# Kernel tuning notes

Hardware: AMD Instinct MI355X
Metric: run time of the kernel (lower is better)

## Reference

```python
import math
import jax, jax.numpy as jnp
import numpy as np

B, N1, N2 = 4, 1024, 768
DIM, H, DK = 1536, 8, 64
DV = DIM // H          # 192
NRPF = DIM // H        # 192, divisible by 6
ESM_CELL = 1280 + 256  # 1536
LN_EPS = 1e-5


def layer_norm(t, g, b):
    mu = jnp.mean(t, axis=-1, keepdims=True)
    var = jnp.mean(jnp.square(t - mu), axis=-1, keepdims=True)
    return (t - mu) * jax.lax.rsqrt(var + LN_EPS) * g + b


def positional_embed(n, feature_size):
    # Enformer-style relative positional features for distances -n+1..n-1
    distances = jnp.arange(-n + 1, n, dtype=jnp.float32)  # [2n-1]
    absd = jnp.abs(distances)[:, None]
    nb = feature_size // 6  # 3 basis fns x 2 (sym + signed)
    seq_len = float(n)
    # exponential
    max_range = math.log(seq_len) / math.log(2.0)
    half_life = 2.0 ** jnp.linspace(3.0, max_range, nb)
    f_exp = jnp.exp(-math.log(2.0) / half_life * absd)
    # central mask
    widths = 2.0 ** jnp.arange(1, nb + 1, dtype=jnp.float32) - 1.0
    f_cm = (widths[None, :] > absd).astype(jnp.float32)
    # gamma pdf
    stddev = seq_len / (2.0 * nb)
    start_mean = seq_len / nb
    mean = jnp.linspace(start_mean, seq_len, nb)
    conc = (mean / stddev) ** 2
    rate = mean / stddev ** 2
    log_p = jax.scipy.special.xlogy(conc - 1.0, absd) - rate * absd
    log_norm = jax.scipy.special.gammaln(conc) - conc * jnp.log(rate)
    prob = jnp.exp(log_p - log_norm) + 1e-8
    f_gam = prob / jnp.max(prob, axis=-1, keepdims=True)
    emb = jnp.concatenate([f_exp, f_cm, f_gam], axis=-1)
    return jnp.concatenate([emb, jnp.sign(distances)[:, None] * emb], axis=-1)  # [2n-1, feature_size]


def relative_shift(x):
    # x: [b, h, t1, 2n-1] -> [b, h, t1, n]
    b, h, t1, _ = x.shape
    x = jnp.pad(x, ((0, 0), (0, 0), (0, 0), (1, 0)))
    t2 = x.shape[-1]  # 2n
    x = x.reshape(b, h, t2, t1)[:, :, 1:, :].reshape(b, h, t1, t2 - 1)
    return x[..., : (t2 + 1) // 2]


def ffn(t, g, b, w1, b1, w2, b2):
    h = layer_norm(t, g, b)
    h = jax.nn.relu(h @ w1 + b1)
    return h @ w2 + b2


def setup_inputs() -> dict:
    key = jax.random.key(0)
    ks = jax.random.split(key, 20)
    s = 0.02
    d = {
        'x': jax.random.normal(ks[0], (B, N1, DIM), jnp.float32),
        'y0': jax.random.normal(ks[1], (B, N2, ESM_CELL), jnp.float32),
        'res_w': jax.random.normal(ks[2], (ESM_CELL, DIM)) * s,
        'lnx_g': jnp.ones((DIM,)), 'lnx_b': jnp.zeros((DIM,)),
        'lny_g': jnp.ones((DIM,)), 'lny_b': jnp.zeros((DIM,)),
        'wq': jax.random.normal(ks[3], (DIM, H * DK)) * s,
        'wk': jax.random.normal(ks[4], (DIM, H * DK)) * s,
        'wv1': jax.random.normal(ks[5], (DIM, H * DV)) * s,
        'wv2': jax.random.normal(ks[6], (DIM, H * DV)) * s,
        'wrel': jax.random.normal(ks[7], (NRPF, H * DK)) * s,
        'rel_pos_bias': jax.random.normal(ks[8], (1, H, 1, DK)),
        'wo1': jax.random.normal(ks[9], (H * DV, DIM)) * s, 'bo1': jnp.zeros((DIM,)),
        'wo2': jax.random.normal(ks[10], (H * DV, DIM)) * s, 'bo2': jnp.zeros((DIM,)),
        'fx_ln_g': jnp.ones((DIM,)), 'fx_ln_b': jnp.zeros((DIM,)),
        'fx_w1': jax.random.normal(ks[11], (DIM, 2 * DIM)) * s, 'fx_b1': jnp.zeros((2 * DIM,)),
        'fx_w2': jax.random.normal(ks[12], (2 * DIM, DIM)) * s, 'fx_b2': jnp.zeros((DIM,)),
        'fy_ln_g': jnp.ones((DIM,)), 'fy_ln_b': jnp.zeros((DIM,)),
        'fy_w1': jax.random.normal(ks[13], (DIM, 2 * DIM)) * s, 'fy_b1': jnp.zeros((2 * DIM,)),
        'fy_w2': jax.random.normal(ks[14], (2 * DIM, DIM)) * s, 'fy_b2': jnp.zeros((DIM,)),
    }
    return d


def reference(x, y0, res_w, lnx_g, lnx_b, lny_g, lny_b, wq, wk, wv1, wv2,
              wrel, rel_pos_bias, wo1, bo1, wo2, bo2,
              fx_ln_g, fx_ln_b, fx_w1, fx_b1, fx_w2, fx_b2,
              fy_ln_g, fy_ln_b, fy_w1, fy_b1, fy_w2, fy_b2):
    scale = DK ** -0.5
    y = y0 @ res_w                                   # res_proj (first layer)
    x1 = layer_norm(x, lnx_g, lnx_b)
    y1 = layer_norm(y, lny_g, lny_b)

    def heads(t, dh):  # [b, n, h*dh] -> [b, h, n, dh]
        return t.reshape(t.shape[0], t.shape[1], H, dh).transpose(0, 2, 1, 3)

    q = heads(x1 @ wq, DK) * scale                   # [b,h,n1,dk]
    k = heads(y1 @ wk, DK)                           # [b,h,n2,dk]
    v2 = heads(y1 @ wv2, DV)                         # [b,h,n2,dv]

    content = jnp.einsum('bhid,bhjd->bhij', q, k)    # [b,h,n1,n2]

    pos = positional_embed(N1, NRPF)                 # [2n1-1, nrpf]
    rel_q = (pos @ wrel).reshape(2 * N1 - 1, H, DK).transpose(1, 0, 2)  # [h,2n1-1,dk]
    rel_logits = jnp.einsum('bhjd,hnd->bhjn', k * scale + rel_pos_bias, rel_q)  # [b,h,n2,2n1-1]
    rel_logits = relative_shift(rel_logits)          # [b,h,n2,n1]
    logits = content + rel_logits.transpose(0, 1, 3, 2)

    attn = jax.nn.softmax(logits, axis=-1)           # [b,h,n1,n2]

    out1 = jnp.einsum('bhij,bhjd->bhid', attn, v2)   # [b,h,n1,dv]
    out1 = out1.transpose(0, 2, 1, 3).reshape(B, N1, H * DV)
    x2 = out1 @ wo1 + bo1

    # exchange branch: reuse attn^T on v1 from stream x
    v1 = heads(x1 @ wv1, DV)                         # [b,h,n1,dv]
    out2 = jnp.einsum('bhij,bhid->bhjd', attn, v1)   # [b,h,n2,dv]
    out2 = out2.transpose(0, 2, 1, 3).reshape(B, N2, H * DV)
    y2 = out2 @ wo2 + bo2

    x4 = x + x2
    x5 = x4 + ffn(x4, fx_ln_g, fx_ln_b, fx_w1, fx_b1, fx_w2, fx_b2)
    y4 = y + y2
    y5 = y4 + ffn(y4, fy_ln_g, fy_ln_b, fy_w1, fy_b1, fy_w2, fy_b2)
    return x5, y5
```

## Files before the change

### kernel.cpp

```cpp
#include <hip/hip_runtime.h>
#include <stdint.h>
#include <math.h>

typedef __attribute__((ext_vector_type(8))) short s8v;
typedef __attribute__((ext_vector_type(4))) short s4v;
typedef __attribute__((ext_vector_type(4))) float f4v;

#define DEV static __device__ __forceinline__

DEV short f2bf(float f) {
  uint32_t u = __builtin_bit_cast(uint32_t, f);
  u += 0x7FFFu + ((u >> 16) & 1u);
  return (short)(u >> 16);
}
DEV float bf2f(short s) {
  uint32_t u = ((uint32_t)(uint16_t)s) << 16;
  return __builtin_bit_cast(float, u);
}

#define GLD16(g, l) __builtin_amdgcn_global_load_lds( \
    (const __attribute__((address_space(1))) void*)(g), \
    (__attribute__((address_space(3))) void*)(l), 16, 0, 0)

__global__ __launch_bounds__(256) void gemm_bt(
    const short* __restrict__ A, const short* __restrict__ B,
    float* Cf, short* Cb,
    const float* __restrict__ bias, const float* resid,
    int M, int N, int K, int lda, int ldb, int ldc,
    long long sAo, long long sAi, long long sBo, long long sBi,
    long long sCo, long long sCi, float alpha, int relu)
{
  __shared__ __align__(16) short lA[128*32];
  __shared__ __align__(16) short lB[128*32];
  const int z = blockIdx.z, zo = z >> 3, zi = z & 7;
  const short* Ab = A + zo*sAo + zi*sAi;
  const short* Bb = B + zo*sBo + zi*sBi;
  const long long cOff = zo*sCo + zi*sCi;

  const int m0 = blockIdx.y*128, n0 = blockIdx.x*128;
  const int tid = threadIdx.x, lane = tid & 63, wv = tid >> 6;
  const int wm = (wv >> 1)*64, wn = (wv & 1)*64;
  const int fr = lane & 15, fq = lane >> 4;

  f4v acc[4][4] = {};

  const int rA0 = min(m0 + (tid >> 2), M - 1);
  const int rA1 = min(m0 + 64 + (tid >> 2), M - 1);
  const int rB0 = min(n0 + (tid >> 2), N - 1);
  const int rB1 = min(n0 + 64 + (tid >> 2), N - 1);
  const int pc = (tid & 3) * 8;
  const short* gA0 = Ab + (size_t)rA0*lda + pc;
  const short* gA1 = Ab + (size_t)rA1*lda + pc;
  const short* gB0 = Bb + (size_t)rB0*ldb + pc;
  const short* gB1 = Bb + (size_t)rB1*ldb + pc;
  short* dA0 = lA + (wv*64)*8;
  short* dA1 = lA + (256 + wv*64)*8;
  short* dB0 = lB + (wv*64)*8;
  short* dB1 = lB + (256 + wv*64)*8;

  for (int k0 = 0; k0 < K; k0 += 32) {
    GLD16(gA0 + k0, dA0);
    GLD16(gA1 + k0, dA1);
    GLD16(gB0 + k0, dB0);
    GLD16(gB1 + k0, dB1);
    __syncthreads();
    s8v af[4], bg[4];
#pragma unroll
    for (int i = 0; i < 4; i++) {
      af[i] = *(const s8v*)&lA[(wm + i*16 + fr)*32 + fq*8];
      bg[i] = *(const s8v*)&lB[(wn + i*16 + fr)*32 + fq*8];
    }
#pragma unroll
    for (int mi = 0; mi < 4; mi++)
#pragma unroll
      for (int ni = 0; ni < 4; ni++)
        acc[mi][ni] = __builtin_amdgcn_mfma_f32_16x16x32_bf16(af[mi], bg[ni], acc[mi][ni], 0, 0, 0);
    __syncthreads();
  }

#pragma unroll
  for (int mi = 0; mi < 4; mi++) {
    const int row = m0 + wm + mi*16 + fq*4;
#pragma unroll
    for (int ni = 0; ni < 4; ni++) {
      const int col = n0 + wn + ni*16 + fr;
      if (col >= N) continue;
      const float bv = bias ? bias[col] : 0.f;
#pragma unroll
      for (int r = 0; r < 4; r++) {
        if (row + r >= M) continue;
        float v = acc[mi][ni][r] * alpha + bv;
        const long long idx = cOff + (long long)(row + r)*ldc + col;
        if (resid) v += resid[idx];
        if (relu) v = fmaxf(v, 0.f);
        if (Cf) Cf[idx] = v;
        if (Cb) Cb[idx] = f2bf(v);
      }
    }
  }
}

#define ST_A(buf, ks, tt) do { const int ko = ((tt)<<6) + ((ks)<<5); \
    GLD16(gA0 + ko, ldA + ((buf)*2+(ks))*8192); \
    GLD16(gA1 + ko, ldA + ((buf)*2+(ks))*8192 + 4096); } while(0)
#define ST_B(buf, ks, tt) do { const int ko = ((tt)<<6) + ((ks)<<5); \
    GLD16(gB0 + ko, ldB + ((buf)*2+(ks))*8192); \
    GLD16(gB1 + ko, ldB + ((buf)*2+(ks))*8192 + 4096); } while(0)

#define PH256(buf, ks, mig, READB, DOWAIT, ...) do { \
    s8v av[4]; \
    const int rb = ((buf)*2+(ks))*8192; \
    _Pragma("unroll") for (int q2 = 0; q2 < 4; q2++) av[q2] = *(const s8v*)&smem[rb + aoff[(mig)*4+q2]]; \
    if (READB) { _Pragma("unroll") for (int q2 = 0; q2 < 4; q2++) bv[q2] = *(const s8v*)&smem[32768 + rb + boff[q2]]; } \
    __VA_ARGS__; \
    if (DOWAIT == 1) asm volatile("s_waitcnt vmcnt(6)" ::: "memory"); \
    if (DOWAIT == 2) asm volatile("s_waitcnt vmcnt(0)" ::: "memory"); \
    __builtin_amdgcn_s_barrier(); \
    asm volatile("s_waitcnt lgkmcnt(0)" ::: "memory"); \
    __builtin_amdgcn_s_setprio(1); \
    _Pragma("unroll") for (int q2 = 0; q2 < 4; q2++) \
      _Pragma("unroll") for (int u2 = 0; u2 < 4; u2++) \
        acc[(mig)*4+q2][u2] = __builtin_amdgcn_mfma_f32_16x16x32_bf16(av[q2], bv[u2], acc[(mig)*4+q2][u2], 0, 0, 0); \
    __builtin_amdgcn_s_setprio(0); \
  } while(0)

__global__ __launch_bounds__(512, 2) void gemm256(
    const short* __restrict__ A0p, const short* __restrict__ B0p,
    float* C0f, short* C0b, const float* __restrict__ bias0, const float* res0,
    int nb0, int nbm0, int N0, float al0,
    const short* __restrict__ A1p, const short* __restrict__ B1p,
    float* C1f, short* C1b, const float* __restrict__ bias1, const float* res1,
    int nbm1, int N1, float al1,
    int K, int relu)
{
  __shared__ __align__(16) short smem[65536];
  const int total = gridDim.x;
  int bid = blockIdx.x;
  if ((total & 7) == 0) bid = (bid & 7)*(total >> 3) + (bid >> 3);
  const short* A; const short* B; float* Cf; short* Cb; const float* bias; const float* resid;
  int tile, nbm, N; float alpha;
  if (bid < nb0) { A = A0p; B = B0p; Cf = C0f; Cb = C0b; bias = bias0; resid = res0;
                   tile = bid; nbm = nbm0; N = N0; alpha = al0; }
  else           { A = A1p; B = B1p; Cf = C1f; Cb = C1b; bias = bias1; resid = res1;
                   tile = bid - nb0; nbm = nbm1; N = N1; alpha = al1; }
  const int bm = tile % nbm, bn = tile / nbm;
  const int m0 = bm << 8, n0 = bn << 8;
  const int t = threadIdx.x, lane = t & 63, w = t >> 6;
  const int wm = w >> 2, wn = w & 3;
  const int fr = lane & 15, fq = lane >> 4;
  const int ntk = K >> 6;

  const int r0 = t >> 2, r1 = 128 + (t >> 2), gsw = t & 3;
  const int cs0 = (gsw ^ ((r0 >> 1) & 3)) << 3;
  const int cs1 = (gsw ^ ((r1 >> 1) & 3)) << 3;
  const short* gA0 = A + (size_t)(m0 + r0)*K + cs0;
  const short* gA1 = A + (size_t)(m0 + r1)*K + cs1;
  const short* gB0 = B + (size_t)(n0 + r0)*K + cs0;
  const short* gB1 = B + (size_t)(n0 + r1)*K + cs1;
  short* const ldA = smem + w*512;
  short* const ldB = smem + 32768 + w*512;

  int aoff[8], boff[4];
#pragma unroll
  for (int mi = 0; mi < 8; mi++) { const int r = wm*128 + mi*16 + fr; aoff[mi] = r*32 + ((fq ^ ((r >> 1) & 3)) << 3); }
#pragma unroll
  for (int ni = 0; ni < 4; ni++) { const int r = wn*64 + ni*16 + fr; boff[ni] = r*32 + ((fq ^ ((r >> 1) & 3)) << 3); }

  f4v acc[8][4] = {};
  s8v bv[4];

  ST_A(0,0,0); ST_B(0,0,0); ST_A(0,1,0); ST_B(0,1,0);
  ST_B(1,0,1); ST_A(1,0,1); ST_B(1,1,1);
  asm volatile("s_waitcnt vmcnt(6)" ::: "memory");
  __builtin_amdgcn_s_barrier();
  asm volatile("" ::: "memory");

  for (int it = 0, nit = (ntk >> 1) - 1; it < nit; ++it) {
    const int t1 = 2*it + 1, t2 = 2*it + 2, t3 = 2*it + 3;
    PH256(0,0,0, 1,0, ST_A(1,1,t1));
    PH256(0,0,1, 0,0, ST_B(0,0,t2));
    PH256(0,1,0, 1,0, ST_A(0,0,t2));
    PH256(0,1,1, 0,1, ST_B(0,1,t2));
    PH256(1,0,0, 1,0, ST_A(0,1,t2));
    PH256(1,0,1, 0,0, ST_B(1,0,t3));
    PH256(1,1,0, 1,0, ST_A(1,0,t3));
    PH256(1,1,1, 0,1, ST_B(1,1,t3));
  }
  PH256(0,0,0, 1,0, ST_A(1,1,ntk-1));
  PH256(0,0,1, 0,0, );
  PH256(0,1,0, 1,0, );
  PH256(0,1,1, 0,2, );
  PH256(1,0,0, 1,0, );
  PH256(1,0,1, 0,0, );
  PH256(1,1,0, 1,0, );
  PH256(1,1,1, 0,0, );

#pragma unroll
  for (int mi = 0; mi < 8; mi++) {
    const int row = m0 + wm*128 + mi*16 + fq*4;
#pragma unroll
    for (int ni = 0; ni < 4; ni++) {
      const int col = n0 + wn*64 + ni*16 + fr;
      const float bvv = bias ? bias[col] : 0.f;
#pragma unroll
      for (int r = 0; r < 4; r++) {
        float v = acc[mi][ni][r]*alpha + bvv;
        const size_t idx = (size_t)(row + r)*N + col;
        if (resid) v += resid[idx];
        if (relu) v = fmaxf(v, 0.f);
        if (Cf) Cf[idx] = v;
        else Cb[idx] = f2bf(v);
      }
    }
  }
}

__global__ __launch_bounds__(256) void wtrans(const float* __restrict__ src,
                                              short* __restrict__ dst, int R, int C)
{
  __shared__ float t[32][33];
  const int c0 = blockIdx.x*32, r0 = blockIdx.y*32;
  const int tx = threadIdx.x, ty = threadIdx.y;
#pragma unroll
  for (int k = 0; k < 4; k++)
    t[ty + k*8][tx] = src[(size_t)(r0 + ty + k*8)*C + c0 + tx];
  __syncthreads();
#pragma unroll
  for (int k = 0; k < 4; k++)
    dst[(size_t)(c0 + ty + k*8)*R + r0 + tx] = f2bf(t[tx][ty + k*8]);
}

__global__ __launch_bounds__(256) void btrans(const short* __restrict__ src, short* __restrict__ dst,
    int ls, int ld_, long long sSo, long long sSi, long long sDo, long long sDi)
{
  __shared__ short t[32][33];
  const int z = blockIdx.z;
  const short* S = src + (z>>3)*sSo + (z&7)*sSi;
  short* D = dst + (z>>3)*sDo + (z&7)*sDi;
  const int c0 = blockIdx.x*32, r0 = blockIdx.y*32;
  const int tx = threadIdx.x, ty = threadIdx.y;
#pragma unroll
  for (int k = 0; k < 4; k++)
    t[ty + k*8][tx] = S[(size_t)(r0 + ty + k*8)*ls + c0 + tx];
  __syncthreads();
#pragma unroll
  for (int k = 0; k < 4; k++)
    D[(size_t)(c0 + ty + k*8)*ld_ + r0 + tx] = t[tx][ty + k*8];
}

__global__ __launch_bounds__(256) void conv_bf(const float* __restrict__ src,
                                               short* __restrict__ dst, long long n)
{
  const long long i = ((long long)blockIdx.x*256 + threadIdx.x)*4;
  if (i >= n) return;
  const float4 v = *(const float4*)(src + i);
  s4v o = { f2bf(v.x), f2bf(v.y), f2bf(v.z), f2bf(v.w) };
  *(s4v*)(dst + i) = o;
}

__global__ __launch_bounds__(256) void ln_k(const float* __restrict__ in,
    const float* __restrict__ gam, const float* __restrict__ bet, short* __restrict__ out)
{
  const long long row = blockIdx.x;
  const float* r = in + row*1536;
  const int tid = threadIdx.x;
  float v[6], s = 0.f, s2 = 0.f;
#pragma unroll
  for (int i = 0; i < 6; i++) { v[i] = r[tid + i*256]; s += v[i]; s2 += v[i]*v[i]; }
  for (int m = 1; m < 64; m <<= 1) { s += __shfl_xor(s, m); s2 += __shfl_xor(s2, m); }
  __shared__ float rs[4], rs2[4];
  if ((tid & 63) == 0) { rs[tid>>6] = s; rs2[tid>>6] = s2; }
  __syncthreads();
  s = rs[0]+rs[1]+rs[2]+rs[3]; s2 = rs2[0]+rs2[1]+rs2[2]+rs2[3];
  const float mu  = s * (1.f/1536.f);
  const float var = s2 * (1.f/1536.f) - mu*mu;
  const float inv = rsqrtf(var + 1e-5f);
  short* o = out + row*1536;
#pragma unroll
  for (int i = 0; i < 6; i++) { int c = tid + i*256; o[c] = f2bf((v[i]-mu)*inv*gam[c] + bet[c]); }
}

__global__ __launch_bounds__(64) void posemb(short* __restrict__ out)
{
  const int i = blockIdx.x;
  const int j = threadIdx.x;
  const float dist = (float)(i - 1023);
  const float absd = fabsf(dist);
  float fe = 0.f, fc = 0.f, prob = 0.f;
  if (j < 32) {
    const float hl = exp2f(3.f + 7.f*(float)j/31.f);
    fe = expf(-0.6931471805599453f/hl * absd);
    const float width = exp2f((float)(j+1)) - 1.f;
    fc = (width > absd) ? 1.f : 0.f;
    const float m = 32.f*(float)(j+1);
    const float conc = (m/16.f)*(m/16.f);
    const float rate = m/256.f;
    const float logp = (absd > 0.f ? (conc-1.f)*logf(absd) : -INFINITY) - rate*absd;
    const float logn = lgammaf(conc) - conc*logf(rate);
    prob = expf(logp - logn) + 1e-8f;
  }
  float mx = prob;
  for (int m = 1; m < 32; m <<= 1) mx = fmaxf(mx, __shfl_xor(mx, m));
  if (j < 32) {
    const float fg = prob / mx;
    const float sg = dist > 0.f ? 1.f : (dist < 0.f ? -1.f : 0.f);
    const size_t base = (size_t)i*192;
    out[base + j]       = f2bf(fe);
    out[base + 32 + j]  = f2bf(fc);
    out[base + 64 + j]  = f2bf(fg);
    out[base + 96 + j]  = f2bf(sg*fe);
    out[base + 128 + j] = f2bf(sg*fc);
    out[base + 160 + j] = f2bf(sg*fg);
  }
}

__global__ __launch_bounds__(256) void relbias_k(const float* __restrict__ rpb,
    const short* __restrict__ relq, float* __restrict__ T)
{
  const int n = blockIdx.x;
  const int tid = threadIdx.x;
  const int h = tid >> 5, l = tid & 31;
  const int d = l*2;
  float s = rpb[h*64+d]   * bf2f(relq[(size_t)n*512 + h*64 + d])
          + rpb[h*64+d+1] * bf2f(relq[(size_t)n*512 + h*64 + d+1]);
  for (int m = 1; m < 32; m <<= 1) s += __shfl_xor(s, m);
  if (l == 0) T[h*2047 + n] = s;
}

__global__ __launch_bounds__(256) void scores_k(
    const short* __restrict__ qb, const short* __restrict__ kb,
    const short* __restrict__ relq, const float* __restrict__ T,
    float* __restrict__ L)
{
  __shared__ __align__(16) short smem[21504];
  short* kt  = smem;
  short* qt  = smem + 4608;
  short* rqt = smem + 4608;
  float* P   = (float*)(smem + 4608);

  const int z = blockIdx.z, b = z >> 3, h = z & 7;
  const int j0 = blockIdx.x*64, i0 = blockIdx.y*64;
  const int tid = threadIdx.x, lane = tid & 63, wv = tid >> 6;
  const int fr = lane & 15, fq = lane >> 4;

  {
    const short* kg = kb + (size_t)(b*768  + j0)*512 + h*64;
    const short* qg = qb + (size_t)(b*1024 + i0)*512 + h*64;
    for (int c = tid; c < 512; c += 256) {
      const int r = c >> 3, ch = (c & 7)*8;
      *(s8v*)&kt[r*72 + ch] = *(const s8v*)&kg[(size_t)r*512 + ch];
      *(s8v*)&qt[r*72 + ch] = *(const s8v*)&qg[(size_t)r*512 + ch];
    }
  }
  __syncthreads();

  const int wi = (wv & 1)*32, wj = (wv >> 1)*32;
  f4v c2[2][2] = {};
#pragma unroll
  for (int ks = 0; ks < 2; ks++) {
    s8v aq[2], bk[2];
#pragma unroll
    for (int mi = 0; mi < 2; mi++) aq[mi] = *(const s8v*)&qt[(wi + mi*16 + fr)*72 + ks*32 + fq*8];
#pragma unroll
    for (int ni = 0; ni < 2; ni++) bk[ni] = *(const s8v*)&kt[(wj + ni*16 + fr)*72 + ks*32 + fq*8];
#pragma unroll
    for (int mi = 0; mi < 2; mi++)
#pragma unroll
      for (int ni = 0; ni < 2; ni++)
        c2[mi][ni] = __builtin_amdgcn_mfma_f32_16x16x32_bf16(aq[mi], bk[ni], c2[mi][ni], 0, 0, 0);
  }
  __syncthreads();

  const int nbase = 704 + i0 - j0;
  {
    const short* rg = relq + (size_t)nbase*512 + h*64;
    for (int c = tid; c < 1024; c += 256) {
      const int r = c >> 3, ch = (c & 7)*8;
      *(s8v*)&rqt[r*72 + ch] = *(const s8v*)&rg[(size_t)r*512 + ch];
    }
  }
  __syncthreads();

  const int wj2 = (wv & 1)*32, wn2 = (wv >> 1)*64;
  f4v pr[2][4] = {};
#pragma unroll
  for (int ks = 0; ks < 2; ks++) {
    s8v a2[2], b2[4];
#pragma unroll
    for (int mi = 0; mi < 2; mi++) a2[mi] = *(const s8v*)&kt[(wj2 + mi*16 + fr)*72 + ks*32 + fq*8];
#pragma unroll
    for (int ni = 0; ni < 4; ni++) b2[ni] = *(const s8v*)&rqt[(wn2 + ni*16 + fr)*72 + ks*32 + fq*8];
#pragma unroll
    for (int mi = 0; mi < 2; mi++)
#pragma unroll
      for (int ni = 0; ni < 4; ni++)
        pr[mi][ni] = __builtin_amdgcn_mfma_f32_16x16x32_bf16(a2[mi], b2[ni], pr[mi][ni], 0, 0, 0);
  }
  __syncthreads();

#pragma unroll
  for (int mi = 0; mi < 2; mi++)
#pragma unroll
    for (int ni = 0; ni < 4; ni++)
#pragma unroll
      for (int r = 0; r < 4; r++)
        P[(wj2 + mi*16 + fq*4 + r)*132 + wn2 + ni*16 + fr] = pr[mi][ni][r];
  __syncthreads();

  const float* Tt = T + h*2047 + nbase;
  float* Lb = L + ((size_t)z*1024 + i0)*768 + j0;
#pragma unroll
  for (int mi = 0; mi < 2; mi++)
#pragma unroll
    for (int ni = 0; ni < 2; ni++)
#pragma unroll
      for (int r = 0; r < 4; r++) {
        const int il = wi + mi*16 + fq*4 + r;
        const int jl = wj + ni*16 + fr;
        const int nl = 63 + il - jl;
        Lb[(size_t)il*768 + jl] = c2[mi][ni][r] + 0.125f*P[jl*132 + nl] + Tt[nl];
      }
}

__global__ __launch_bounds__(256) void softmax_k(const float* __restrict__ L, short* __restrict__ P)
{
  const long long row = blockIdx.x;
  const float* r = L + row*768;
  const int tid = threadIdx.x;
  float v0 = r[tid], v1 = r[tid+256], v2 = r[tid+512];
  float mx = fmaxf(v0, fmaxf(v1, v2));
  for (int m = 1; m < 64; m <<= 1) mx = fmaxf(mx, __shfl_xor(mx, m));
  __shared__ float redm[4], reds[4];
  if ((tid & 63) == 0) redm[tid>>6] = mx;
  __syncthreads();
  mx = fmaxf(fmaxf(redm[0], redm[1]), fmaxf(redm[2], redm[3]));
  v0 = __expf(v0 - mx); v1 = __expf(v1 - mx); v2 = __expf(v2 - mx);
  float s = v0 + v1 + v2;
  for (int m = 1; m < 64; m <<= 1) s += __shfl_xor(s, m);
  if ((tid & 63) == 0) reds[tid>>6] = s;
  __syncthreads();
  s = reds[0] + reds[1] + reds[2] + reds[3];
  const float inv = 1.f / s;
  short* o = P + row*768;
  o[tid] = f2bf(v0*inv); o[tid+256] = f2bf(v1*inv); o[tid+512] = f2bf(v2*inv);
}

static void gemm(hipStream_t st, const short* A, const short* B, float* Cf, short* Cb,
                 const float* bias, const float* resid,
                 int M, int N, int K, int lda, int ldb, int ldc,
                 int batches = 1,
                 long long sAo = 0, long long sAi = 0, long long sBo = 0, long long sBi = 0,
                 long long sCo = 0, long long sCi = 0, float alpha = 1.f, int relu = 0)
{
  dim3 g((N + 127)/128, (M + 127)/128, batches);
  gemm_bt<<<g, dim3(256), 0, st>>>(A, B, Cf, Cb, bias, resid, M, N, K, lda, ldb, ldc,
                                   sAo, sAi, sBo, sBi, sCo, sCi, alpha, relu);
}

static void g256(hipStream_t st,
    const short* A0, const short* B0, float* C0f, short* C0b, const float* bias0, const float* res0,
    int M0, int N0, float al0,
    const short* A1, const short* B1, float* C1f, short* C1b, const float* bias1, const float* res1,
    int M1, int N1, float al1,
    int K, int relu)
{
  const int nbm0 = M0 >> 8, nbn0 = N0 >> 8, nb0 = nbm0*nbn0;
  const int nbm1 = M1 >> 8, nbn1 = N1 >> 8, nb1 = nbm1*nbn1;
  gemm256<<<dim3(nb0 + nb1), dim3(512), 0, st>>>(
      A0, B0, C0f, C0b, bias0, res0, nb0, nbm0, N0, al0,
      A1, B1, C1f, C1b, bias1, res1, nbm1, N1, al1, K, relu);
}

extern "C" void kernel_launch(void* const* d_in, const int* in_sizes, int n_in,
                              void* d_out, int out_size, void* d_ws, size_t ws_size,
                              hipStream_t stream)
{
  (void)in_sizes; (void)n_in; (void)out_size; (void)ws_size;
  const float* x     = (const float*)d_in[0];
  const float* y0    = (const float*)d_in[1];
  const float* lnxg  = (const float*)d_in[3];
  const float* lnxb  = (const float*)d_in[4];
  const float* lnyg  = (const float*)d_in[5];
  const float* lnyb  = (const float*)d_in[6];
  const float* rpb   = (const float*)d_in[12];
  const float* bo1   = (const float*)d_in[14];
  const float* bo2   = (const float*)d_in[16];
  const float* fxg   = (const float*)d_in[17];
  const float* fxbb  = (const float*)d_in[18];
  const float* fxb1  = (const float*)d_in[20];
  const float* fxb2  = (const float*)d_in[22];
  const float* fyg   = (const float*)d_in[23];
  const float* fybb  = (const float*)d_in[24];
  const float* fyb1  = (const float*)d_in[26];
  const float* fyb2  = (const float*)d_in[28];

  char* base = (char*)d_ws;
  size_t off = 0;
  auto bump = [&](size_t b) -> char* { char* p = base + off; off += (b + 255) & ~(size_t)255; return p; };

  short* W_A = (short*)bump(4718592);
  short* W_B = (short*)bump(1572864);
  short* W_C = (short*)bump(4718592);
  short* W_D = (short*)bump(196608);
  short* W_E = (short*)bump(9437184);
  short* W_F = (short*)bump(9437184);

  char*  uB = bump(12582912);  short* x1 = (short*)uB;   short* out1 = (short*)uB;
  char*  uC = bump(9437184);   short* y1 = (short*)uC;   short* out2 = (short*)uC;
  char*  uD = bump(9437184);
  short* y0b = (short*)uD;
  short* qb  = (short*)uD;
  short* kbB = (short*)(uD + 4194304);
  float* Tbl   = (float*)bump(262016);
  short* posb  = (short*)bump(786048);
  short* relqb = (short*)bump(2096128);
  char*  uG = bump(12582912);  short* v1b = (short*)uG;  short* x4ln = (short*)uG;
  char*  uH = bump(9437184);   short* v2b = (short*)uH;  short* y4ln = (short*)uH;
  char*  uI = bump(100663296);
  short* wv2T   = (short*)uI;
  float* logits = (float*)uI;
  short* attnT  = (short*)uI;
  short* v1T    = (short*)(uI + 50331648);
  short* v2T    = (short*)(uI + 62914560);
  short* hx     = (short*)uI;
  short* hy     = (short*)(uI + 25165824);
  short* fy1T   = (short*)(uI + 46137344);
  short* fy2T   = (short*)(uI + 55574528);
  char*  U2 = bump(50331648);
  short* attnb = (short*)U2;
  float* y4    = (float*)U2;

  float* outx = (float*)d_out;
  float* outy = (float*)d_out + 6291456;
  float* x4  = outx;
  float* y_f = outy;

  auto WT = [&](int idx, short* dst, int R, int C) {
    wtrans<<<dim3(C/32, R/32), dim3(32,8), 0, stream>>>((const float*)d_in[idx], dst, R, C);
  };

  WT(2,  W_A, 1536, 1536);
  WT(11, W_D, 192,  512);
  WT(9,  W_C, 1536, 1536);
  WT(10, wv2T, 1536, 1536);
  WT(7,  W_B, 1536, 512);
  WT(19, W_E, 1536, 3072);
  WT(21, W_F, 3072, 1536);
  conv_bf<<<4608, 256, 0, stream>>>(y0, y0b, 4718592LL);
  posemb<<<2047, 64, 0, stream>>>(posb);
  gemm(stream, posb, W_D, nullptr, relqb, nullptr, nullptr, 2047, 512, 192, 192, 192, 512);
  relbias_k<<<2047, 256, 0, stream>>>(rpb, relqb, Tbl);
  ln_k<<<4096, 256, 0, stream>>>(x, lnxg, lnxb, x1);
  g256(stream, y0b, W_A, y_f, nullptr, nullptr, nullptr, 3072, 1536, 1.f,
       x1, W_C, nullptr, v1b, nullptr, nullptr, 4096, 1536, 1.f, 1536, 0);
  ln_k<<<3072, 256, 0, stream>>>(y_f, lnyg, lnyb, y1);
  g256(stream, y1, wv2T, nullptr, v2b, nullptr, nullptr, 3072, 1536, 1.f,
       x1, W_B, nullptr, qb, nullptr, nullptr, 4096, 512, 0.125f, 1536, 0);
  WT(8, W_B, 1536, 512);
  gemm(stream, y1, W_B, nullptr, kbB, nullptr, nullptr, 3072, 512, 1536, 1536, 1536, 512);
  WT(13, W_A, 1536, 1536);
  WT(15, W_C, 1536, 1536);
  scores_k<<<dim3(12,16,32), 256, 0, stream>>>(qb, kbB, relqb, Tbl, logits);
  softmax_k<<<32768, 256, 0, stream>>>(logits, attnb);
  btrans<<<dim3(24,32,32), dim3(32,8), 0, stream>>>(attnb, attnT, 768, 1024,
       8LL*786432, 786432, 8LL*786432, 786432);
  btrans<<<dim3(6,32,32), dim3(32,8), 0, stream>>>(v1b, v1T, 1536, 1024,
       1024LL*1536, 192, 8LL*196608, 196608);
  btrans<<<dim3(6,24,32), dim3(32,8), 0, stream>>>(v2b, v2T, 1536, 768,
       768LL*1536, 192, 8LL*147456, 147456);
  gemm(stream, attnb, v2T, nullptr, out1, nullptr, nullptr, 1024, 192, 768, 768, 768, 1536,
       32, 8LL*786432, 786432, 8LL*147456, 147456, 1024LL*1536, 192);
  gemm(stream, attnT, v1T, nullptr, out2, nullptr, nullptr, 768, 192, 1024, 1024, 1024, 1536,
       32, 8LL*786432, 786432, 8LL*196608, 196608, 768LL*1536, 192);
  WT(25, fy1T, 1536, 3072);
  WT(27, fy2T, 3072, 1536);
  g256(stream, out1, W_A, x4, nullptr, bo1, x, 4096, 1536, 1.f,
       out2, W_C, y4, nullptr, bo2, y_f, 3072, 1536, 1.f, 1536, 0);
  ln_k<<<4096, 256, 0, stream>>>(x4, fxg, fxbb, x4ln);
  ln_k<<<3072, 256, 0, stream>>>(y4, fyg, fybb, y4ln);
  g256(stream, x4ln, W_E, nullptr, hx, fxb1, nullptr, 4096, 3072, 1.f,
       y4ln, fy1T, nullptr, hy, fyb1, nullptr, 3072, 3072, 1.f, 1536, 1);
  g256(stream, hx, W_F, outx, nullptr, fxb2, x4, 4096, 1536, 1.f,
       hy, fy2T, outy, nullptr, fyb2, y4, 3072, 1536, 1.f, 3072, 0);
}
```

Before: 761.6 us.

## Fold K projection into grouped 256-tile GEMM and add post-MFMA barrier

The grouped 256x256 GEMM kernel now takes a third problem, so the K projection (y1 @ wk) runs in the same launch as the V2 and Q projections. Previously it ran as a separate 128-tile GEMM, and its weight transpose sat between those launches. The transposed wk weight now gets its own buffer and is prepared up front. Each MFMA phase also gains a sched_barrier and a trailing s_barrier, which is likely a correctness guard against LDS buffer reuse. The extra barrier per phase may add synchronization cost to every GEMM.

```diff
diff --git a/kernel.cpp b/kernel.cpp
--- a/kernel.cpp
+++ b/kernel.cpp
@@ -117,11 +117,14 @@
     if (DOWAIT == 2) asm volatile("s_waitcnt vmcnt(0)" ::: "memory"); \
     __builtin_amdgcn_s_barrier(); \
     asm volatile("s_waitcnt lgkmcnt(0)" ::: "memory"); \
+    __builtin_amdgcn_sched_barrier(0); \
     __builtin_amdgcn_s_setprio(1); \
     _Pragma("unroll") for (int q2 = 0; q2 < 4; q2++) \
       _Pragma("unroll") for (int u2 = 0; u2 < 4; u2++) \
         acc[(mig)*4+q2][u2] = __builtin_amdgcn_mfma_f32_16x16x32_bf16(av[q2], bv[u2], acc[(mig)*4+q2][u2], 0, 0, 0); \
     __builtin_amdgcn_s_setprio(0); \
+    __builtin_amdgcn_s_barrier(); \
+    asm volatile("" ::: "memory"); \
   } while(0)
 
 __global__ __launch_bounds__(512, 2) void gemm256(
@@ -130,7 +133,10 @@
     int nb0, int nbm0, int N0, float al0,
     const short* __restrict__ A1p, const short* __restrict__ B1p,
     float* C1f, short* C1b, const float* __restrict__ bias1, const float* res1,
-    int nbm1, int N1, float al1,
+    int nb01, int nbm1, int N1, float al1,
+    const short* __restrict__ A2p, const short* __restrict__ B2p,
+    float* C2f, short* C2b, const float* __restrict__ bias2, const float* res2,
+    int nbm2, int N2, float al2,
     int K, int relu)
 {
   __shared__ __align__(16) short smem[65536];
@@ -139,10 +145,12 @@
   if ((total & 7) == 0) bid = (bid & 7)*(total >> 3) + (bid >> 3);
   const short* A; const short* B; float* Cf; short* Cb; const float* bias; const float* resid;
   int tile, nbm, N; float alpha;
-  if (bid < nb0) { A = A0p; B = B0p; Cf = C0f; Cb = C0b; bias = bias0; resid = res0;
-                   tile = bid; nbm = nbm0; N = N0; alpha = al0; }
-  else           { A = A1p; B = B1p; Cf = C1f; Cb = C1b; bias = bias1; resid = res1;
-                   tile = bid - nb0; nbm = nbm1; N = N1; alpha = al1; }
+  if (bid < nb0)       { A = A0p; B = B0p; Cf = C0f; Cb = C0b; bias = bias0; resid = res0;
+                         tile = bid; nbm = nbm0; N = N0; alpha = al0; }
+  else if (bid < nb01) { A = A1p; B = B1p; Cf = C1f; Cb = C1b; bias = bias1; resid = res1;
+                         tile = bid - nb0; nbm = nbm1; N = N1; alpha = al1; }
+  else                 { A = A2p; B = B2p; Cf = C2f; Cb = C2b; bias = bias2; resid = res2;
+                         tile = bid - nb01; nbm = nbm2; N = N2; alpha = al2; }
   const int bm = tile % nbm, bn = tile / nbm;
   const int m0 = bm << 8, n0 = bn << 8;
   const int t = threadIdx.x, lane = t & 63, w = t >> 6;
@@ -457,6 +465,24 @@
                                    sAo, sAi, sBo, sBi, sCo, sCi, alpha, relu);
 }
 
+static void g256_3(hipStream_t st,
+    const short* A0, const short* B0, float* C0f, short* C0b, const float* bias0, const float* res0,
+    int M0, int N0, float al0,
+    const short* A1, const short* B1, float* C1f, short* C1b, const float* bias1, const float* res1,
+    int M1, int N1, float al1,
+    const short* A2, const short* B2, float* C2f, short* C2b, const float* bias2, const float* res2,
+    int M2, int N2, float al2,
+    int K, int relu)
+{
+  const int nbm0 = M0 >> 8, nb0 = nbm0*(N0 >> 8);
+  const int nbm1 = M1 >> 8, nb1 = nbm1*(N1 >> 8);
+  const int nbm2 = M2 >> 8, nb2 = M2 ? nbm2*(N2 >> 8) : 0;
+  gemm256<<<dim3(nb0 + nb1 + nb2), dim3(512), 0, st>>>(
+      A0, B0, C0f, C0b, bias0, res0, nb0, nbm0, N0, al0,
+      A1, B1, C1f, C1b, bias1, res1, nb0 + nb1, nbm1, N1, al1,
+      A2, B2, C2f, C2b, bias2, res2, nbm2, N2, al2, K, relu);
+}
+
 static void g256(hipStream_t st,
     const short* A0, const short* B0, float* C0f, short* C0b, const float* bias0, const float* res0,
     int M0, int N0, float al0,
@@ -464,11 +490,9 @@
     int M1, int N1, float al1,
     int K, int relu)
 {
-  const int nbm0 = M0 >> 8, nbn0 = N0 >> 8, nb0 = nbm0*nbn0;
-  const int nbm1 = M1 >> 8, nbn1 = N1 >> 8, nb1 = nbm1*nbn1;
-  gemm256<<<dim3(nb0 + nb1), dim3(512), 0, st>>>(
-      A0, B0, C0f, C0b, bias0, res0, nb0, nbm0, N0, al0,
-      A1, B1, C1f, C1b, bias1, res1, nbm1, N1, al1, K, relu);
+  g256_3(st, A0, B0, C0f, C0b, bias0, res0, M0, N0, al0,
+         A1, B1, C1f, C1b, bias1, res1, M1, N1, al1,
+         nullptr, nullptr, nullptr, nullptr, nullptr, nullptr, 0, 256, 1.f, K, relu);
 }
 
 extern "C" void kernel_launch(void* const* d_in, const int* in_sizes, int n_in,
@@ -498,12 +522,13 @@
   size_t off = 0;
   auto bump = [&](size_t b) -> char* { char* p = base + off; off += (b + 255) & ~(size_t)255; return p; };
 
-  short* W_A = (short*)bump(4718592);
-  short* W_B = (short*)bump(1572864);
-  short* W_C = (short*)bump(4718592);
-  short* W_D = (short*)bump(196608);
-  short* W_E = (short*)bump(9437184);
-  short* W_F = (short*)bump(9437184);
+  short* W_A  = (short*)bump(4718592);
+  short* W_B  = (short*)bump(1572864);
+  short* W_B2 = (short*)bump(1572864);
+  short* W_C  = (short*)bump(4718592);
+  short* W_D  = (short*)bump(196608);
+  short* W_E  = (short*)bump(9437184);
+  short* W_F  = (short*)bump(9437184);
 
   char*  uB = bump(12582912);  short* x1 = (short*)uB;   short* out1 = (short*)uB;
   char*  uC = bump(9437184);   short* y1 = (short*)uC;   short* out2 = (short*)uC;
@@ -544,6 +569,7 @@
   WT(9,  W_C, 1536, 1536);
   WT(10, wv2T, 1536, 1536);
   WT(7,  W_B, 1536, 512);
+  WT(8,  W_B2, 1536, 512);
   WT(19, W_E, 1536, 3072);
   WT(21, W_F, 3072, 1536);
   conv_bf<<<4608, 256, 0, stream>>>(y0, y0b, 4718592LL);
@@ -554,10 +580,9 @@
   g256(stream, y0b, W_A, y_f, nullptr, nullptr, nullptr, 3072, 1536, 1.f,
        x1, W_C, nullptr, v1b, nullptr, nullptr, 4096, 1536, 1.f, 1536, 0);
   ln_k<<<3072, 256, 0, stream>>>(y_f, lnyg, lnyb, y1);
-  g256(stream, y1, wv2T, nullptr, v2b, nullptr, nullptr, 3072, 1536, 1.f,
-       x1, W_B, nullptr, qb, nullptr, nullptr, 4096, 512, 0.125f, 1536, 0);
-  WT(8, W_B, 1536, 512);
-  gemm(stream, y1, W_B, nullptr, kbB, nullptr, nullptr, 3072, 512, 1536, 1536, 1536, 512);
+  g256_3(stream, y1, wv2T, nullptr, v2b, nullptr, nullptr, 3072, 1536, 1.f,
+         x1, W_B, nullptr, qb, nullptr, nullptr, 4096, 512, 0.125f,
+         y1, W_B2, nullptr, kbB, nullptr, nullptr, 3072, 512, 1.f, 1536, 0);
   WT(13, W_A, 1536, 1536);
   WT(15, W_C, 1536, 1536);
   scores_k<<<dim3(12,16,32), 256, 0, stream>>>(qb, kbB, relqb, Tbl, logits);
```

Result: faster. 732.7 us (-3.8%).
